# Optimization experiments

Hardware: AMD Instinct MI355X
Metric: run time of the kernel (lower is better)

The kernel has to match this reference:

```python
import jax, jax.numpy as jnp
import numpy as np

NUM_CLASSES = 1000  # label vocabulary size (matches fill_max for label)
B = 16384
D_IN = 1024   # image_embedding
D_OUT = 256   # projection_dim


def setup_inputs() -> dict:
    key = jax.random.key(0)
    k = jax.random.split(key, 6)
    x = jax.random.normal(k[0], (B, D_IN), dtype=jnp.float32)
    label = jax.random.randint(k[1], (B,), 0, NUM_CLASSES, dtype=jnp.int64)
    scale = 1.0 / np.sqrt(D_IN)
    W1_w = jax.random.normal(k[2], (D_OUT, D_IN), dtype=jnp.float32) * scale
    W1_b = jax.random.normal(k[3], (D_OUT,), dtype=jnp.float32) * scale
    W2_w = jax.random.normal(k[4], (D_OUT, D_IN), dtype=jnp.float32) * scale
    W2_b = jax.random.normal(k[5], (D_OUT,), dtype=jnp.float32) * scale
    return {"x": x, "label": label, "W1_w": W1_w, "W1_b": W1_b,
            "W2_w": W2_w, "W2_b": W2_b}


def reference(x, label, W1_w, W1_b, W2_w, W2_b):
    # Leave-one-group-out mean, vectorized via segment sums.
    # Original: for each i, mean of x[label != label_i] (detached); zeros if none.
    b = x.shape[0]
    xd = jax.lax.stop_gradient(x)  # .detach() in the torch code
    label_sum = jax.ops.segment_sum(xd, label, num_segments=NUM_CLASSES)          # [C, D_IN]
    label_cnt = jax.ops.segment_sum(jnp.ones((b,), dtype=x.dtype), label,
                                    num_segments=NUM_CLASSES)                     # [C]
    total_sum = xd.sum(axis=0)                                                    # [D_IN]
    other_sum = total_sum[None, :] - label_sum[label]                             # [B, D_IN]
    other_cnt = jnp.asarray(b, x.dtype) - label_cnt[label]                        # [B]
    calculate_mean = jnp.where(other_cnt[:, None] > 0,
                               other_sum / jnp.maximum(other_cnt, 1)[:, None],
                               jnp.zeros((), x.dtype))                            # [B, D_IN]
    # W1(x) + W2(calculate_mean)  (torch Linear: y = x @ W.T + b)
    return x @ W1_w.T + W1_b + calculate_mean @ W2_w.T + W2_b
```

## Files before the change

kernel.cpp:

```cpp
#include <hip/hip_runtime.h>
#include <hip/hip_bf16.h>

constexpr int B      = 16384;
constexpr int D_IN   = 1024;
constexpr int D_OUT  = 256;
constexpr int NCLS   = 1000;
constexpr int CPAD   = 1024;

constexpr size_t OFF_XB   = 0;
constexpr size_t OFF_WB   = OFF_XB  + (size_t)B * D_IN * 2;
constexpr size_t OFF_S    = OFF_WB  + (size_t)512 * D_IN * 2;
constexpr size_t OFF_Z    = OFF_S   + (size_t)CPAD * D_IN * 4;
constexpr size_t OFF_T    = OFF_Z   + (size_t)CPAD * D_OUT * 4;
constexpr size_t OFF_CNT  = OFF_T   + (size_t)D_IN * 4;
constexpr size_t OFF_OFFS = OFF_CNT + (size_t)CPAD * 4;
constexpr size_t OFF_CUR  = OFF_OFFS+ (size_t)CPAD * 4;
constexpr size_t OFF_ROWL = OFF_CUR + (size_t)CPAD * 4;

typedef short bf16x8 __attribute__((ext_vector_type(8)));
typedef float f32x4  __attribute__((ext_vector_type(4)));

__device__ __forceinline__ unsigned short f2bf(float f) {
    unsigned int u = __float_as_uint(f);
    return (unsigned short)((u + 0x7FFFu + ((u >> 16) & 1u)) >> 16);
}

__device__ __forceinline__ void cvt8(const float4& a, const float4& b, unsigned short* dst) {
    union { unsigned short u[8]; bf16x8 v; } r;
    r.u[0] = f2bf(a.x); r.u[1] = f2bf(a.y); r.u[2] = f2bf(a.z); r.u[3] = f2bf(a.w);
    r.u[4] = f2bf(b.x); r.u[5] = f2bf(b.y); r.u[6] = f2bf(b.z); r.u[7] = f2bf(b.w);
    *(bf16x8*)dst = r.v;
}

__device__ __forceinline__ ushort4 f2bf4(const float4& a) {
    ushort4 r;
    r.x = f2bf(a.x); r.y = f2bf(a.y); r.z = f2bf(a.z); r.w = f2bf(a.w);
    return r;
}

__device__ __forceinline__ void async16(const unsigned short* g, unsigned short* l) {
    __builtin_amdgcn_global_load_lds(
        (const __attribute__((address_space(1))) void*)g,
        (__attribute__((address_space(3))) void*)l,
        16, 0, 0);
}

__global__ __launch_bounds__(1024)
void prep_kernel(const float* __restrict__ W1, const float* __restrict__ W2,
                 unsigned short* __restrict__ Wb,
                 float* __restrict__ T, float* __restrict__ Z,
                 const int* __restrict__ label,
                 int* __restrict__ cnt, int* __restrict__ offs,
                 int* __restrict__ rowlist) {
    __shared__ int hA[1024];
    __shared__ int hB[1024];

    if (blockIdx.x < 64) {
        int lin = blockIdx.x * 1024 + threadIdx.x;
        int i = lin * 8;
        const float* src = (i < D_OUT * D_IN) ? (W1 + i) : (W2 + (i - D_OUT * D_IN));
        float4 a = *(const float4*)(src);
        float4 b = *(const float4*)(src + 4);
        cvt8(a, b, Wb + i);
        if (lin < D_IN) T[lin] = 0.f;
        *(float4*)(Z + (size_t)lin * 4) = float4{0.f, 0.f, 0.f, 0.f};
        return;
    }

    int t = threadIdx.x;
    hA[t] = 0;
    __syncthreads();
    int lab[16];
#pragma unroll
    for (int r = 0; r < 16; ++r) {
        lab[r] = label[t + r * 1024];
        atomicAdd(&hA[lab[r]], 1);
    }
    __syncthreads();
    int v = hA[t];
    int* src = hA;
    int* dst = hB;
    for (int off = 1; off < 1024; off <<= 1) {
        int sv = src[t];
        if (t >= off) sv += src[t - off];
        dst[t] = sv;
        __syncthreads();
        int* tmp = src; src = dst; dst = tmp;
    }
    int excl = src[t] - v;
    cnt[t]  = v;
    offs[t] = excl;
    dst[t]  = excl;
    __syncthreads();
#pragma unroll
    for (int r = 0; r < 16; ++r) {
        int p = atomicAdd(&dst[lab[r]], 1);
        rowlist[p] = t + r * 1024;
    }
}

__global__ void segsum_kernel(const float* __restrict__ x,
                              const int* __restrict__ offs,
                              const int* __restrict__ cnt,
                              const int* __restrict__ rowlist,
                              float* __restrict__ s,
                              unsigned short* __restrict__ xb) {
    int c = blockIdx.x;
    int col = threadIdx.x * 4;
    float4 acc = {0.f, 0.f, 0.f, 0.f};
    if (c < NCLS) {
        int o = offs[c], n = cnt[c];
        int r = 0;
        for (; r + 8 <= n; r += 8) {
            int idx[8];
#pragma unroll
            for (int u = 0; u < 8; ++u) idx[u] = rowlist[o + r + u];
            float4 v[8];
#pragma unroll
            for (int u = 0; u < 8; ++u)
                v[u] = *(const float4*)(x + (size_t)idx[u] * D_IN + col);
#pragma unroll
            for (int u = 0; u < 8; ++u)
                *(ushort4*)(xb + (size_t)idx[u] * D_IN + col) = f2bf4(v[u]);
#pragma unroll
            for (int u = 0; u < 8; ++u) {
                acc.x += v[u].x; acc.y += v[u].y; acc.z += v[u].z; acc.w += v[u].w;
            }
        }
        for (; r + 4 <= n; r += 4) {
            int i0 = rowlist[o + r + 0];
            int i1 = rowlist[o + r + 1];
            int i2 = rowlist[o + r + 2];
            int i3 = rowlist[o + r + 3];
            float4 v0 = *(const float4*)(x + (size_t)i0 * D_IN + col);
            float4 v1 = *(const float4*)(x + (size_t)i1 * D_IN + col);
            float4 v2 = *(const float4*)(x + (size_t)i2 * D_IN + col);
            float4 v3 = *(const float4*)(x + (size_t)i3 * D_IN + col);
            *(ushort4*)(xb + (size_t)i0 * D_IN + col) = f2bf4(v0);
            *(ushort4*)(xb + (size_t)i1 * D_IN + col) = f2bf4(v1);
            *(ushort4*)(xb + (size_t)i2 * D_IN + col) = f2bf4(v2);
            *(ushort4*)(xb + (size_t)i3 * D_IN + col) = f2bf4(v3);
            acc.x += (v0.x + v1.x) + (v2.x + v3.x);
            acc.y += (v0.y + v1.y) + (v2.y + v3.y);
            acc.z += (v0.z + v1.z) + (v2.z + v3.z);
            acc.w += (v0.w + v1.w) + (v2.w + v3.w);
        }
        for (; r < n; ++r) {
            int i0 = rowlist[o + r];
            float4 v = *(const float4*)(x + (size_t)i0 * D_IN + col);
            *(ushort4*)(xb + (size_t)i0 * D_IN + col) = f2bf4(v);
            acc.x += v.x; acc.y += v.y; acc.z += v.z; acc.w += v.w;
        }
    }
    *(float4*)(s + (size_t)c * D_IN + col) = acc;
}

__global__ void tsum_kernel(const float* __restrict__ s, float* __restrict__ T) {
    int col = threadIdx.x * 4;
    int c0 = blockIdx.x * 16;
    float4 acc = {0.f, 0.f, 0.f, 0.f};
#pragma unroll 4
    for (int c = 0; c < 16; ++c) {
        float4 v = *(const float4*)(s + (size_t)(c0 + c) * D_IN + col);
        acc.x += v.x; acc.y += v.y; acc.z += v.z; acc.w += v.w;
    }
    atomicAdd(&T[col + 0], acc.x);
    atomicAdd(&T[col + 1], acc.y);
    atomicAdd(&T[col + 2], acc.z);
    atomicAdd(&T[col + 3], acc.w);
}

__global__ __launch_bounds__(256)
void meanz_kernel(const float* __restrict__ s,
                  const float* __restrict__ T,
                  const int* __restrict__ cnt,
                  const unsigned short* __restrict__ Wb,
                  const float* __restrict__ b2,
                  float* __restrict__ Z) {
    __shared__ unsigned short As[64 * 32];
    __shared__ unsigned short Bs[64 * 32];

    const int tid  = threadIdx.x;
    const int wave = tid >> 6;
    const int lane = tid & 63;
    const int quad = lane >> 4;
    const int l16  = lane & 15;
    const int bm   = blockIdx.x * 64;
    const int bn   = blockIdx.y * 64;
    const int kb   = blockIdx.z * 256;
    const int wm   = (wave >> 1) * 32;
    const int wn   = (wave & 1) * 32;

    const int arow = tid >> 2;
    const int akc  = (tid & 3) * 8;

    const int cls = bm + arow;
    const int d   = B - cnt[cls];
    const float scale = (d > 0) ? 1.f / (float)d : 0.f;
    const float* sp = s + (size_t)cls * D_IN + akc;
    const float* tp = T + akc;

    const int bidx = wave * 64 + lane;
    const int brow = bidx >> 2;
    const int bkc  = (bidx & 3) * 8;
    const unsigned short* bp = Wb + (size_t)(256 + bn + brow) * D_IN + bkc;

    f32x4 acc[2][2] = {};

    for (int k0 = kb; k0 < kb + 256; k0 += 32) {
        float4 s0 = *(const float4*)(sp + k0);
        float4 s1 = *(const float4*)(sp + k0 + 4);
        float4 t0 = *(const float4*)(tp + k0);
        float4 t1 = *(const float4*)(tp + k0 + 4);
        __syncthreads();
        async16(bp + k0, Bs + wave * 512);
        float4 m0 = {(t0.x - s0.x) * scale, (t0.y - s0.y) * scale,
                     (t0.z - s0.z) * scale, (t0.w - s0.w) * scale};
        float4 m1 = {(t1.x - s1.x) * scale, (t1.y - s1.y) * scale,
                     (t1.z - s1.z) * scale, (t1.w - s1.w) * scale};
        cvt8(m0, m1, As + arow * 32 + akc);
        __syncthreads();

        bf16x8 af[2], bfr[2];
#pragma unroll
        for (int t = 0; t < 2; ++t) {
            af[t]  = *(const bf16x8*)&As[(wm + t * 16 + l16) * 32 + quad * 8];
            bfr[t] = *(const bf16x8*)&Bs[(wn + t * 16 + l16) * 32 + quad * 8];
        }
#pragma unroll
        for (int i = 0; i < 2; ++i)
#pragma unroll
            for (int j = 0; j < 2; ++j)
                acc[i][j] = __builtin_amdgcn_mfma_f32_16x16x32_bf16(af[i], bfr[j], acc[i][j], 0, 0, 0);
    }

    const bool addb = (blockIdx.z == 0);
#pragma unroll
    for (int j = 0; j < 2; ++j) {
        const int n = bn + wn + j * 16 + l16;
        const float bias = addb ? b2[n] : 0.f;
#pragma unroll
        for (int i = 0; i < 2; ++i)
#pragma unroll
            for (int r = 0; r < 4; ++r) {
                const int c = bm + wm + i * 16 + quad * 4 + r;
                atomicAdd(&Z[(size_t)c * D_OUT + n], acc[i][j][r] + bias);
            }
    }
}

__global__ __launch_bounds__(256)
void gemm1_kernel(const unsigned short* __restrict__ xb,
                  const unsigned short* __restrict__ Wb,
                  const float* __restrict__ b1,
                  const float* __restrict__ Z,
                  const int* __restrict__ label,
                  float* __restrict__ out) {
    __shared__ unsigned short As[2][128][32];
    __shared__ unsigned short Bs[2][64][32];

    const int tid  = threadIdx.x;
    const int wave = tid >> 6;
    const int lane = tid & 63;
    const int quad = lane >> 4;
    const int l16  = lane & 15;
    const int bm   = blockIdx.x * 128;
    const int bn   = blockIdx.y * 64;
    const int wm   = (wave >> 1) * 64;
    const int wn   = (wave & 1) * 32;

    const unsigned short* aps[4];
#pragma unroll
    for (int rr = 0; rr < 4; ++rr) {
        int dd = rr * 256 + tid;
        int h = dd >> 9, r = (dd >> 2) & 127, c = dd & 3;
        aps[rr] = xb + (size_t)(bm + r) * D_IN + h * 32 + c * 8;
    }
    const unsigned short* bps[2];
#pragma unroll
    for (int rr = 0; rr < 2; ++rr) {
        int dd = rr * 256 + tid;
        int h = dd >> 8, r = (dd >> 2) & 63, c = dd & 3;
        bps[rr] = Wb + (size_t)(bn + r) * D_IN + h * 32 + c * 8;
    }

    f32x4 acc[4][2] = {};

    for (int k0 = 0; k0 < D_IN; k0 += 64) {
        __syncthreads();
#pragma unroll
        for (int rr = 0; rr < 4; ++rr)
            async16(aps[rr] + k0, &As[0][0][0] + rr * 2048 + wave * 512);
#pragma unroll
        for (int rr = 0; rr < 2; ++rr)
            async16(bps[rr] + k0, &Bs[0][0][0] + rr * 2048 + wave * 512);
        __syncthreads();

#pragma unroll
        for (int ks = 0; ks < 2; ++ks) {
            bf16x8 af[4], bfr[2];
#pragma unroll
            for (int i = 0; i < 4; ++i)
                af[i] = *(const bf16x8*)&As[ks][wm + i * 16 + l16][quad * 8];
#pragma unroll
            for (int j = 0; j < 2; ++j)
                bfr[j] = *(const bf16x8*)&Bs[ks][wn + j * 16 + l16][quad * 8];
#pragma unroll
            for (int i = 0; i < 4; ++i)
#pragma unroll
                for (int j = 0; j < 2; ++j)
                    acc[i][j] = __builtin_amdgcn_mfma_f32_16x16x32_bf16(af[i], bfr[j], acc[i][j], 0, 0, 0);
        }
    }

    int zrow[4][4];
#pragma unroll
    for (int i = 0; i < 4; ++i)
#pragma unroll
        for (int r = 0; r < 4; ++r)
            zrow[i][r] = label[bm + wm + i * 16 + quad * 4 + r] * D_OUT;

#pragma unroll
    for (int j = 0; j < 2; ++j) {
        const int n = bn + wn + j * 16 + l16;
        const float bias = b1[n];
#pragma unroll
        for (int i = 0; i < 4; ++i)
#pragma unroll
            for (int r = 0; r < 4; ++r) {
                const int m = bm + wm + i * 16 + quad * 4 + r;
                out[(size_t)m * D_OUT + n] = acc[i][j][r] + bias + Z[zrow[i][r] + n];
            }
    }
}

extern "C" void kernel_launch(void* const* d_in, const int* in_sizes, int n_in,
                              void* d_out, int out_size, void* d_ws, size_t ws_size,
                              hipStream_t stream) {
    const float* x    = (const float*)d_in[0];
    const int*   lab  = (const int*)d_in[1];
    const float* W1_w = (const float*)d_in[2];
    const float* W1_b = (const float*)d_in[3];
    const float* W2_w = (const float*)d_in[4];
    const float* W2_b = (const float*)d_in[5];
    float* out = (float*)d_out;

    char* ws = (char*)d_ws;
    unsigned short* xb = (unsigned short*)(ws + OFF_XB);
    unsigned short* Wb = (unsigned short*)(ws + OFF_WB);
    float* s   = (float*)(ws + OFF_S);
    float* Z   = (float*)(ws + OFF_Z);
    float* T   = (float*)(ws + OFF_T);
    int* cnt     = (int*)(ws + OFF_CNT);
    int* offs    = (int*)(ws + OFF_OFFS);
    int* rowlist = (int*)(ws + OFF_ROWL);

    prep_kernel<<<65, 1024, 0, stream>>>(W1_w, W2_w, Wb, T, Z, lab, cnt, offs, rowlist);
    segsum_kernel<<<CPAD, 256, 0, stream>>>(x, offs, cnt, rowlist, s, xb);
    tsum_kernel<<<64, 256, 0, stream>>>(s, T);
    dim3 zgrid(CPAD / 64, D_OUT / 64, 4);
    meanz_kernel<<<zgrid, 256, 0, stream>>>(s, T, cnt, Wb, W2_b, Z);
    dim3 ggrid(B / 128, D_OUT / 64);
    gemm1_kernel<<<ggrid, 256, 0, stream>>>(xb, Wb, W1_b, Z, lab, out);
}
```

Measured before the change: 163.8 us.

## Double-buffer LDS tiles in both GEMMs and split segsum columns across blocks

Adds double-buffered shared-memory tiles to gemm1 and meanz so the async loads for the next K-step are issued while MFMAs run on the current buffer, and each iteration needs one barrier instead of two. The segsum kernel is split across two column halves with 128-thread blocks to double the grid size and improve occupancy on the gather/convert pass. This is meant to hide global-load latency behind compute, at the cost of doubling LDS use per block, which may lower the number of resident blocks. It also relies on the async copies being complete when the barrier is reached.

```diff
diff --git a/kernel.cpp b/kernel.cpp
--- a/kernel.cpp
+++ b/kernel.cpp
@@ -99,14 +99,15 @@
     }
 }
 
-__global__ void segsum_kernel(const float* __restrict__ x,
-                              const int* __restrict__ offs,
-                              const int* __restrict__ cnt,
-                              const int* __restrict__ rowlist,
-                              float* __restrict__ s,
-                              unsigned short* __restrict__ xb) {
+__global__ __launch_bounds__(128)
+void segsum_kernel(const float* __restrict__ x,
+                   const int* __restrict__ offs,
+                   const int* __restrict__ cnt,
+                   const int* __restrict__ rowlist,
+                   float* __restrict__ s,
+                   unsigned short* __restrict__ xb) {
     int c = blockIdx.x;
-    int col = threadIdx.x * 4;
+    int col = blockIdx.y * 512 + threadIdx.x * 4;
     float4 acc = {0.f, 0.f, 0.f, 0.f};
     if (c < NCLS) {
         int o = offs[c], n = cnt[c];
@@ -177,8 +178,8 @@
                   const unsigned short* __restrict__ Wb,
                   const float* __restrict__ b2,
                   float* __restrict__ Z) {
-    __shared__ unsigned short As[64 * 32];
-    __shared__ unsigned short Bs[64 * 32];
+    __shared__ unsigned short As[2][64 * 32];
+    __shared__ unsigned short Bs[2][64 * 32];
 
     const int tid  = threadIdx.x;
     const int wave = tid >> 6;
@@ -207,25 +208,34 @@
 
     f32x4 acc[2][2] = {};
 
-    for (int k0 = kb; k0 < kb + 256; k0 += 32) {
-        float4 s0 = *(const float4*)(sp + k0);
-        float4 s1 = *(const float4*)(sp + k0 + 4);
-        float4 t0 = *(const float4*)(tp + k0);
-        float4 t1 = *(const float4*)(tp + k0 + 4);
+    float4 cs0 = *(const float4*)(sp + kb);
+    float4 cs1 = *(const float4*)(sp + kb + 4);
+    float4 ct0 = *(const float4*)(tp + kb);
+    float4 ct1 = *(const float4*)(tp + kb + 4);
+    async16(bp + kb, Bs[0] + wave * 512);
+
+    for (int it = 0; it < 8; ++it) {
+        const int cur = it & 1;
+        const int k0  = kb + it * 32;
+        float4 m0 = {(ct0.x - cs0.x) * scale, (ct0.y - cs0.y) * scale,
+                     (ct0.z - cs0.z) * scale, (ct0.w - cs0.w) * scale};
+        float4 m1 = {(ct1.x - cs1.x) * scale, (ct1.y - cs1.y) * scale,
+                     (ct1.z - cs1.z) * scale, (ct1.w - cs1.w) * scale};
+        cvt8(m0, m1, As[cur] + arow * 32 + akc);
+        if (it < 7) {
+            async16(bp + k0 + 32, Bs[cur ^ 1] + wave * 512);
+            cs0 = *(const float4*)(sp + k0 + 32);
+            cs1 = *(const float4*)(sp + k0 + 36);
+            ct0 = *(const float4*)(tp + k0 + 32);
+            ct1 = *(const float4*)(tp + k0 + 36);
+        }
         __syncthreads();
-        async16(bp + k0, Bs + wave * 512);
-        float4 m0 = {(t0.x - s0.x) * scale, (t0.y - s0.y) * scale,
-                     (t0.z - s0.z) * scale, (t0.w - s0.w) * scale};
-        float4 m1 = {(t1.x - s1.x) * scale, (t1.y - s1.y) * scale,
-                     (t1.z - s1.z) * scale, (t1.w - s1.w) * scale};
-        cvt8(m0, m1, As + arow * 32 + akc);
-        __syncthreads();
 
         bf16x8 af[2], bfr[2];
 #pragma unroll
         for (int t = 0; t < 2; ++t) {
-            af[t]  = *(const bf16x8*)&As[(wm + t * 16 + l16) * 32 + quad * 8];
-            bfr[t] = *(const bf16x8*)&Bs[(wn + t * 16 + l16) * 32 + quad * 8];
+            af[t]  = *(const bf16x8*)&As[cur][(wm + t * 16 + l16) * 32 + quad * 8];
+            bfr[t] = *(const bf16x8*)&Bs[cur][(wn + t * 16 + l16) * 32 + quad * 8];
         }
 #pragma unroll
         for (int i = 0; i < 2; ++i)
@@ -256,8 +266,8 @@
                   const float* __restrict__ Z,
                   const int* __restrict__ label,
                   float* __restrict__ out) {
-    __shared__ unsigned short As[2][128][32];
-    __shared__ unsigned short Bs[2][64][32];
+    __shared__ unsigned short As[2][2][128][32];
+    __shared__ unsigned short Bs[2][2][64][32];
 
     const int tid  = threadIdx.x;
     const int wave = tid >> 6;
@@ -286,31 +296,44 @@
 
     f32x4 acc[4][2] = {};
 
-    for (int k0 = 0; k0 < D_IN; k0 += 64) {
-        __syncthreads();
-#pragma unroll
-        for (int rr = 0; rr < 4; ++rr)
-            async16(aps[rr] + k0, &As[0][0][0] + rr * 2048 + wave * 512);
-#pragma unroll
-        for (int rr = 0; rr < 2; ++rr)
-            async16(bps[rr] + k0, &Bs[0][0][0] + rr * 2048 + wave * 512);
-        __syncthreads();
+    {
+        unsigned short* ab = &As[0][0][0][0];
+        unsigned short* bb = &Bs[0][0][0][0];
+#pragma unroll
+        for (int rr = 0; rr < 4; ++rr) async16(aps[rr], ab + rr * 2048 + wave * 512);
+#pragma unroll
+        for (int rr = 0; rr < 2; ++rr) async16(bps[rr], bb + rr * 2048 + wave * 512);
+    }
+    __syncthreads();
+
+    for (int t = 0; t < 16; ++t) {
+        const int cur = t & 1;
+        if (t + 1 < 16) {
+            const int k1 = (t + 1) * 64;
+            unsigned short* ab = &As[cur ^ 1][0][0][0];
+            unsigned short* bb = &Bs[cur ^ 1][0][0][0];
+#pragma unroll
+            for (int rr = 0; rr < 4; ++rr) async16(aps[rr] + k1, ab + rr * 2048 + wave * 512);
+#pragma unroll
+            for (int rr = 0; rr < 2; ++rr) async16(bps[rr] + k1, bb + rr * 2048 + wave * 512);
+        }
 
 #pragma unroll
         for (int ks = 0; ks < 2; ++ks) {
             bf16x8 af[4], bfr[2];
 #pragma unroll
             for (int i = 0; i < 4; ++i)
-                af[i] = *(const bf16x8*)&As[ks][wm + i * 16 + l16][quad * 8];
+                af[i] = *(const bf16x8*)&As[cur][ks][wm + i * 16 + l16][quad * 8];
 #pragma unroll
             for (int j = 0; j < 2; ++j)
-                bfr[j] = *(const bf16x8*)&Bs[ks][wn + j * 16 + l16][quad * 8];
+                bfr[j] = *(const bf16x8*)&Bs[cur][ks][wn + j * 16 + l16][quad * 8];
 #pragma unroll
             for (int i = 0; i < 4; ++i)
 #pragma unroll
                 for (int j = 0; j < 2; ++j)
                     acc[i][j] = __builtin_amdgcn_mfma_f32_16x16x32_bf16(af[i], bfr[j], acc[i][j], 0, 0, 0);
         }
+        __syncthreads();
     }
 
     int zrow[4][4];
@@ -356,7 +379,8 @@
     int* rowlist = (int*)(ws + OFF_ROWL);
 
     prep_kernel<<<65, 1024, 0, stream>>>(W1_w, W2_w, Wb, T, Z, lab, cnt, offs, rowlist);
-    segsum_kernel<<<CPAD, 256, 0, stream>>>(x, offs, cnt, rowlist, s, xb);
+    dim3 sgrid(CPAD, 2);
+    segsum_kernel<<<sgrid, 128, 0, stream>>>(x, offs, cnt, rowlist, s, xb);
     tsum_kernel<<<64, 256, 0, stream>>>(s, T);
     dim3 zgrid(CPAD / 64, D_OUT / 64, 4);
     meanz_kernel<<<zgrid, 256, 0, stream>>>(s, T, cnt, Wb, W2_b, Z);
```

New measurement: 164.4 us. No clear change (+0.3%).
